# Kernel optimization log

Measured on AMD Instinct MI355X. Metric: run time of the kernel, lower is better.

The kernel has to match this reference:

```python
import jax, jax.numpy as jnp
import numpy as np

N_NODES = 100000
N_EDGES = 1600000
D = 128  # in_features


def setup_inputs() -> dict:
    key = jax.random.key(0)
    k1, k2, k3 = jax.random.split(key, 3)
    node_embeddings = jax.random.normal(k1, (N_NODES, D), dtype=jnp.float32)
    edge_index = jax.random.randint(k2, (2, N_EDGES), 0, N_NODES, dtype=jnp.int64)
    # attn_fc: Linear(2*D, 2) -> weight [2, 2*D], bias [2]
    W = jax.random.normal(k3, (2, 2 * D), dtype=jnp.float32) * (1.0 / np.sqrt(2 * D))
    b = jnp.zeros((2,), dtype=jnp.float32)
    return {"node_embeddings": node_embeddings, "edge_index": edge_index, "W": W, "b": b}


def reference(node_embeddings, edge_index, W, b):
    # Gather endpoint embeddings per edge, concat -> [E, 2*D]
    row, col = edge_index[0], edge_index[1]
    edge_feature = jnp.concatenate(
        [node_embeddings[row], node_embeddings[col]], axis=-1
    )  # [E, 2D]
    attn_scores = edge_feature @ W.T + b  # [E, 2]
    attn_scores = jax.nn.softmax(attn_scores, axis=-1)
    # dropout is identity in eval mode
    return attn_scores
```

## Files before the change

### kernel.cpp

```cpp
#include <hip/hip_runtime.h>

static constexpr int kNodes = 100000;
static constexpr int kEdges = 1600000;
static constexpr int kD     = 128;

__global__ __launch_bounds__(64) void detect_idx(const unsigned long long* __restrict__ ei,
                                                 int* __restrict__ flag) {
    if (threadIdx.x == 0 && blockIdx.x == 0) {
        unsigned long long orr = 0ull;
        for (int i = 0; i < 256; ++i) orr |= (ei[i] >> 32);
        *flag = (orr == 0ull) ? 1 : 0;
    }
}

__global__ __launch_bounds__(256) void node_pre(const float* __restrict__ emb,
                                                const float* __restrict__ W,
                                                float* __restrict__ h) {
    const int lane16 = threadIdx.x & 15;
    const int c0 = lane16 * 8;

    float w0[8], w1[8], w2[8], w3[8];
#pragma unroll
    for (int k = 0; k < 8; ++k) {
        w0[k] = W[c0 + k];
        w1[k] = W[256 + c0 + k];
        w2[k] = W[128 + c0 + k];
        w3[k] = W[384 + c0 + k];
    }

    const int group   = (blockIdx.x * blockDim.x + threadIdx.x) >> 4;
    const int ngroups = (gridDim.x * blockDim.x) >> 4;

    for (int n = group; n < kNodes; n += ngroups) {
        const float4* row = (const float4*)(emb + (size_t)n * kD + c0);
        float4 ea = row[0];
        float4 eb = row[1];
        float e[8] = {ea.x, ea.y, ea.z, ea.w, eb.x, eb.y, eb.z, eb.w};
        float p0 = 0.f, p1 = 0.f, p2 = 0.f, p3 = 0.f;
#pragma unroll
        for (int k = 0; k < 8; ++k) {
            p0 += e[k] * w0[k];
            p1 += e[k] * w1[k];
            p2 += e[k] * w2[k];
            p3 += e[k] * w3[k];
        }
#pragma unroll
        for (int m = 1; m < 16; m <<= 1) {
            p0 += __shfl_xor(p0, m, 64);
            p1 += __shfl_xor(p1, m, 64);
            p2 += __shfl_xor(p2, m, 64);
            p3 += __shfl_xor(p3, m, 64);
        }
        if (lane16 == 0) {
            ((float4*)h)[n] = make_float4(p0, p1, p2, p3);
        }
    }
}

__global__ __launch_bounds__(256) void edge_attn(const void* __restrict__ eiv,
                                                 const float* __restrict__ h,
                                                 const float* __restrict__ b,
                                                 const int* __restrict__ flag,
                                                 float* __restrict__ out) {
    const int e = blockIdx.x * blockDim.x + threadIdx.x;
    if (e >= kEdges) return;

    int r, c;
    if (*flag) {
        const long long* ei = (const long long*)eiv;
        r = (int)ei[e];
        c = (int)ei[kEdges + e];
    } else {
        const int* ei = (const int*)eiv;
        r = ei[e];
        c = ei[kEdges + e];
    }

    float4 hr = ((const float4*)h)[r];
    float4 hc = ((const float4*)h)[c];

    const float b0 = b[0], b1 = b[1];
    float s0 = hr.x + hc.z + b0;
    float s1 = hr.y + hc.w + b1;
    float m  = fmaxf(s0, s1);
    float x0 = __expf(s0 - m);
    float x1 = __expf(s1 - m);
    float inv = 1.0f / (x0 + x1);
    ((float2*)out)[e] = make_float2(x0 * inv, x1 * inv);
}

extern "C" void kernel_launch(void* const* d_in, const int* in_sizes, int n_in,
                              void* d_out, int out_size, void* d_ws, size_t ws_size,
                              hipStream_t stream) {
    const float* emb = (const float*)d_in[0];
    const void*  ei  = d_in[1];
    const float* W   = (const float*)d_in[2];
    const float* b   = (const float*)d_in[3];
    float* out = (float*)d_out;

    int*   flag = (int*)d_ws;
    float* h    = (float*)((char*)d_ws + 256);

    detect_idx<<<1, 64, 0, stream>>>((const unsigned long long*)ei, flag);

    node_pre<<<(kNodes * 16 + 255) / 256, 256, 0, stream>>>(emb, W, h);

    edge_attn<<<(kEdges + 255) / 256, 256, 0, stream>>>(ei, h, b, flag, out);
}
```

Measured before the change: 36.88 us.

## Drop detect kernel, vectorize edge kernel to four edges per thread

Removes the separate index-width detection kernel and instead detects int64 vs int32 inline via a wavefront ballot in each block. The edge kernel now handles four edges per thread with vectorized nontemporal index loads and output stores. The node pre-pass uses a shuffle-transpose reduction and runs with a quarter of the grid, looping over nodes. These cut one launch, instruction overhead and cache pollution, at the cost of every block re-reading the first 64 index words and lower parallelism in the node pass.

```diff
diff --git a/kernel.cpp b/kernel.cpp
--- a/kernel.cpp
+++ b/kernel.cpp
@@ -4,89 +4,107 @@
 static constexpr int kEdges = 1600000;
 static constexpr int kD     = 128;
 
-__global__ __launch_bounds__(64) void detect_idx(const unsigned long long* __restrict__ ei,
-                                                 int* __restrict__ flag) {
-    if (threadIdx.x == 0 && blockIdx.x == 0) {
-        unsigned long long orr = 0ull;
-        for (int i = 0; i < 256; ++i) orr |= (ei[i] >> 32);
-        *flag = (orr == 0ull) ? 1 : 0;
-    }
-}
+typedef float              fx4  __attribute__((ext_vector_type(4)));
+typedef int                ix4  __attribute__((ext_vector_type(4)));
+typedef unsigned long long ux2  __attribute__((ext_vector_type(2)));
 
 __global__ __launch_bounds__(256) void node_pre(const float* __restrict__ emb,
                                                 const float* __restrict__ W,
                                                 float* __restrict__ h) {
-    const int lane16 = threadIdx.x & 15;
-    const int c0 = lane16 * 8;
+    const int l  = threadIdx.x & 15;
+    const int c0 = l * 8;
 
-    float w0[8], w1[8], w2[8], w3[8];
-#pragma unroll
-    for (int k = 0; k < 8; ++k) {
-        w0[k] = W[c0 + k];
-        w1[k] = W[256 + c0 + k];
-        w2[k] = W[128 + c0 + k];
-        w3[k] = W[384 + c0 + k];
-    }
+    fx4 w0a = *(const fx4*)&W[c0],       w0b = *(const fx4*)&W[c0 + 4];
+    fx4 w1a = *(const fx4*)&W[256 + c0], w1b = *(const fx4*)&W[256 + c0 + 4];
+    fx4 w2a = *(const fx4*)&W[128 + c0], w2b = *(const fx4*)&W[128 + c0 + 4];
+    fx4 w3a = *(const fx4*)&W[384 + c0], w3b = *(const fx4*)&W[384 + c0 + 4];
 
     const int group   = (blockIdx.x * blockDim.x + threadIdx.x) >> 4;
     const int ngroups = (gridDim.x * blockDim.x) >> 4;
 
     for (int n = group; n < kNodes; n += ngroups) {
-        const float4* row = (const float4*)(emb + (size_t)n * kD + c0);
-        float4 ea = row[0];
-        float4 eb = row[1];
-        float e[8] = {ea.x, ea.y, ea.z, ea.w, eb.x, eb.y, eb.z, eb.w};
-        float p0 = 0.f, p1 = 0.f, p2 = 0.f, p3 = 0.f;
-#pragma unroll
-        for (int k = 0; k < 8; ++k) {
-            p0 += e[k] * w0[k];
-            p1 += e[k] * w1[k];
-            p2 += e[k] * w2[k];
-            p3 += e[k] * w3[k];
-        }
-#pragma unroll
-        for (int m = 1; m < 16; m <<= 1) {
-            p0 += __shfl_xor(p0, m, 64);
-            p1 += __shfl_xor(p1, m, 64);
-            p2 += __shfl_xor(p2, m, 64);
-            p3 += __shfl_xor(p3, m, 64);
-        }
-        if (lane16 == 0) {
-            ((float4*)h)[n] = make_float4(p0, p1, p2, p3);
-        }
+        const fx4* row = (const fx4*)(emb + (size_t)n * kD + c0);
+        fx4 ea = __builtin_nontemporal_load(row);
+        fx4 eb = __builtin_nontemporal_load(row + 1);
+
+        float p0 = ea.x*w0a.x + ea.y*w0a.y + ea.z*w0a.z + ea.w*w0a.w
+                 + eb.x*w0b.x + eb.y*w0b.y + eb.z*w0b.z + eb.w*w0b.w;
+        float p1 = ea.x*w1a.x + ea.y*w1a.y + ea.z*w1a.z + ea.w*w1a.w
+                 + eb.x*w1b.x + eb.y*w1b.y + eb.z*w1b.z + eb.w*w1b.w;
+        float p2 = ea.x*w2a.x + ea.y*w2a.y + ea.z*w2a.z + ea.w*w2a.w
+                 + eb.x*w2b.x + eb.y*w2b.y + eb.z*w2b.z + eb.w*w2b.w;
+        float p3 = ea.x*w3a.x + ea.y*w3a.y + ea.z*w3a.z + ea.w*w3a.w
+                 + eb.x*w3b.x + eb.y*w3b.y + eb.z*w3b.z + eb.w*w3b.w;
+
+        float sendU = (l & 1) ? p0 : p1;
+        float keepU = (l & 1) ? p1 : p0;
+        float u = keepU + __shfl_xor(sendU, 1);
+        float sendW = (l & 1) ? p2 : p3;
+        float keepW = (l & 1) ? p3 : p2;
+        float w = keepW + __shfl_xor(sendW, 1);
+        float sendX = (l & 2) ? u : w;
+        float keepX = (l & 2) ? w : u;
+        float x = keepX + __shfl_xor(sendX, 2);
+        x += __shfl_xor(x, 4);
+        x += __shfl_xor(x, 8);
+
+        if (l < 4) h[n * 4 + l] = x;
     }
 }
 
 __global__ __launch_bounds__(256) void edge_attn(const void* __restrict__ eiv,
                                                  const float* __restrict__ h,
                                                  const float* __restrict__ b,
-                                                 const int* __restrict__ flag,
                                                  float* __restrict__ out) {
-    const int e = blockIdx.x * blockDim.x + threadIdx.x;
-    if (e >= kEdges) return;
+    const unsigned long long* ei64 = (const unsigned long long*)eiv;
+    unsigned long long hi = ei64[threadIdx.x & 63] >> 32;
+    const bool is64 = (__ballot(hi != 0ull) == 0ull);
 
-    int r, c;
-    if (*flag) {
-        const long long* ei = (const long long*)eiv;
-        r = (int)ei[e];
-        c = (int)ei[kEdges + e];
+    const int e4 = blockIdx.x * blockDim.x + threadIdx.x;
+    if (e4 >= kEdges / 4) return;
+
+    int r[4], c[4];
+    if (is64) {
+        const ux2* rr = (const ux2*)ei64;
+        const ux2* cc = (const ux2*)(ei64 + kEdges);
+        ux2 ra = __builtin_nontemporal_load(&rr[2 * e4]);
+        ux2 rb = __builtin_nontemporal_load(&rr[2 * e4 + 1]);
+        ux2 ca = __builtin_nontemporal_load(&cc[2 * e4]);
+        ux2 cb = __builtin_nontemporal_load(&cc[2 * e4 + 1]);
+        r[0] = (int)ra.x; r[1] = (int)ra.y; r[2] = (int)rb.x; r[3] = (int)rb.y;
+        c[0] = (int)ca.x; c[1] = (int)ca.y; c[2] = (int)cb.x; c[3] = (int)cb.y;
     } else {
-        const int* ei = (const int*)eiv;
-        r = ei[e];
-        c = ei[kEdges + e];
+        const ix4* rr = (const ix4*)eiv;
+        const ix4* cc = (const ix4*)((const int*)eiv + kEdges);
+        ix4 ra = __builtin_nontemporal_load(&rr[e4]);
+        ix4 ca = __builtin_nontemporal_load(&cc[e4]);
+        r[0] = ra.x; r[1] = ra.y; r[2] = ra.z; r[3] = ra.w;
+        c[0] = ca.x; c[1] = ca.y; c[2] = ca.z; c[3] = ca.w;
     }
 
-    float4 hr = ((const float4*)h)[r];
-    float4 hc = ((const float4*)h)[c];
+    const fx4* h4 = (const fx4*)h;
+    const float b0 = b[0], b1 = b[1];
 
-    const float b0 = b[0], b1 = b[1];
-    float s0 = hr.x + hc.z + b0;
-    float s1 = hr.y + hc.w + b1;
-    float m  = fmaxf(s0, s1);
-    float x0 = __expf(s0 - m);
-    float x1 = __expf(s1 - m);
-    float inv = 1.0f / (x0 + x1);
-    ((float2*)out)[e] = make_float2(x0 * inv, x1 * inv);
+    float res[8];
+#pragma unroll
+    for (int k = 0; k < 4; ++k) {
+        fx4 hr = h4[r[k]];
+        fx4 hc = h4[c[k]];
+        float s0 = hr.x + hc.z + b0;
+        float s1 = hr.y + hc.w + b1;
+        float m  = fmaxf(s0, s1);
+        float x0 = __expf(s0 - m);
+        float x1 = __expf(s1 - m);
+        float inv = 1.0f / (x0 + x1);
+        res[2*k]     = x0 * inv;
+        res[2*k + 1] = x1 * inv;
+    }
+
+    fx4* o4 = (fx4*)out;
+    fx4 oa = {res[0], res[1], res[2], res[3]};
+    fx4 ob = {res[4], res[5], res[6], res[7]};
+    __builtin_nontemporal_store(oa, &o4[2 * e4]);
+    __builtin_nontemporal_store(ob, &o4[2 * e4 + 1]);
 }
 
 extern "C" void kernel_launch(void* const* d_in, const int* in_sizes, int n_in,
@@ -98,12 +116,9 @@
     const float* b   = (const float*)d_in[3];
     float* out = (float*)d_out;
 
-    int*   flag = (int*)d_ws;
-    float* h    = (float*)((char*)d_ws + 256);
+    float* h = (float*)d_ws;
 
-    detect_idx<<<1, 64, 0, stream>>>((const unsigned long long*)ei, flag);
+    node_pre<<<(kNodes * 16 / 4 + 255) / 256, 256, 0, stream>>>(emb, W, h);
 
-    node_pre<<<(kNodes * 16 + 255) / 256, 256, 0, stream>>>(emb, W, h);
-
-    edge_attn<<<(kEdges + 255) / 256, 256, 0, stream>>>(ei, h, b, flag, out);
+    edge_attn<<<(kEdges / 4 + 255) / 256, 256, 0, stream>>>(ei, h, b, out);
 }
```

After: 36.72 us. Within noise of the previous version (-0.4%).
